# Performance work log

Hardware: AMD Instinct MI355X
Metric: run time of the kernel (lower is better)

The kernel has to match this reference:

```python
import jax, jax.numpy as jnp
import numpy as np

B, T, D, M = 4, 4096, 1024, 1024
EPS = 1e-6


def _rms_norm(x, w):
    return x * jax.lax.rsqrt(jnp.mean(x * x, axis=-1, keepdims=True) + EPS) * w


def _linrec(xg, r, h0):
    # h_t = x_t + r_t * h_{t-1}  (SRU-style linear recurrence, sqrll_kernel)
    def step(h, inp):
        xt, rt = inp
        h = xt + rt * h
        return h, h
    _, ys = jax.lax.scan(step, h0, (jnp.swapaxes(xg, 0, 1), jnp.swapaxes(r, 0, 1)))
    return jnp.swapaxes(ys, 0, 1)  # [B,T,M]


def setup_inputs() -> dict:
    key = jax.random.key(0)
    ks = jax.random.split(key, 16)
    s = 0.02
    return {
        "x": jax.random.normal(ks[0], (B, T, D), jnp.float32),
        "mem": jnp.zeros((B, M), jnp.float32),
        "norm_w": jnp.ones((D,), jnp.float32),
        "wr_w": jax.random.normal(ks[1], (M, D), jnp.float32) * s,
        "wr_b": jnp.zeros((M,), jnp.float32),
        "wi_w": jax.random.normal(ks[2], (M, D), jnp.float32) * s,
        "wig_w": jax.random.normal(ks[3], (M, D), jnp.float32) * s,
        "wig_b": jnp.zeros((M,), jnp.float32),
        "wog_w": jax.random.normal(ks[4], (M, D), jnp.float32) * s,
        "wog_b": jnp.zeros((M,), jnp.float32),
        "wo_w": jax.random.normal(ks[5], (D, M), jnp.float32) * s,
        "ffnorm_w": jnp.ones((D,), jnp.float32),
        "ffn_wi_w": jax.random.normal(ks[6], (M, D), jnp.float32) * s,
        "ffn_wg_w": jax.random.normal(ks[7], (M, D), jnp.float32) * s,
        "ffn_wg_b": jnp.zeros((M,), jnp.float32),
        "ffn_wo_w": jax.random.normal(ks[8], (D, M), jnp.float32) * s,
    }


def reference(x, mem, norm_w, wr_w, wr_b, wi_w, wig_w, wig_b, wog_w, wog_b,
              wo_w, ffnorm_w, ffn_wi_w, ffn_wg_w, ffn_wg_b, ffn_wo_w):
    # --- sqrll branch ---
    y = _rms_norm(x, norm_w)                                   # [B,T,D]
    ig = jax.nn.sigmoid(jnp.einsum('btd,md->btm', y, wig_w) + wig_b)
    og = jax.nn.sigmoid(jnp.einsum('btd,md->btm', y, wog_w) + wog_b)
    r = jax.nn.sigmoid(jnp.einsum('btd,md->btm', y, wr_w) + wr_b)
    xg = jnp.einsum('btd,md->btm', y, wi_w) * ig               # gated input
    h = _linrec(xg, r, mem)                                    # [B,T,M]
    mem_out = jax.lax.stop_gradient(h[:, -1])
    s = (h / (1.0 + jnp.abs(h))) * og                          # softsign * out gate
    x = x + jnp.einsum('btm,dm->btd', s, wo_w)                 # residual (dropout=0)
    # --- gated FFN branch ---
    z = _rms_norm(x, ffnorm_w)
    ff = jnp.einsum('btd,md->btm', z, ffn_wi_w) * jax.nn.sigmoid(
        jnp.einsum('btd,md->btm', z, ffn_wg_w) + ffn_wg_b)
    x = x + jnp.einsum('btm,dm->btd', ff, ffn_wo_w)
    return (x, mem_out)
```

## Files before the change

### kernel.cpp

```cpp
#include <hip/hip_runtime.h>
#include <stdint.h>


#define R_ROWS 16384
#define DIM    1024
#define MDIM   1024
#define TSEQ   4096
#define NCHUNK 128
#define TCH    32

typedef __attribute__((ext_vector_type(8))) short  bf16x8;
typedef __attribute__((ext_vector_type(8))) ushort u16x8;
typedef __attribute__((ext_vector_type(4))) float  f32x4;

__device__ __forceinline__ float bf2f(ushort u) {
  union { float f; unsigned int i; } x; x.i = ((unsigned int)u) << 16; return x.f;
}
__device__ __forceinline__ ushort f2bf(float f) {
  union { float f; unsigned int i; } x; x.f = f;
  unsigned int r = x.i + 0x7fffu + ((x.i >> 16) & 1u);
  return (ushort)(r >> 16);
}
__device__ __forceinline__ float sigmoidf_(float x) {
  return 1.0f / (1.0f + __expf(-x));
}
__device__ __forceinline__ void load_lds16(const void* g, void* s) {
  __builtin_amdgcn_global_load_lds(
      (const __attribute__((address_space(1))) void*)g,
      (__attribute__((address_space(3))) void*)s, 16, 0, 0);
}

__global__ __launch_bounds__(256)
void cvt_weights(const float* __restrict__ w0, const float* __restrict__ w1,
                 const float* __restrict__ w2, const float* __restrict__ w3,
                 const float* __restrict__ w4, const float* __restrict__ w5,
                 const float* __restrict__ w6, ushort* __restrict__ dst)
{
  const float* src;
  switch (blockIdx.y) {
    case 0: src = w0; break; case 1: src = w1; break;
    case 2: src = w2; break; case 3: src = w3; break;
    case 4: src = w4; break; case 5: src = w5; break;
    default: src = w6; break;
  }
  const int i = blockIdx.x * 256 + threadIdx.x;
  const size_t off = (size_t)blockIdx.y * 1048576 + (size_t)i * 4;
  const float4 v = *(const float4*)(src + (size_t)i * 4);
  ushort4 o; o.x = f2bf(v.x); o.y = f2bf(v.y); o.z = f2bf(v.z); o.w = f2bf(v.w);
  *(ushort4*)(dst + off) = o;
}

__global__ __launch_bounds__(256)
void cvt_one(const float* __restrict__ src, ushort* __restrict__ dst)
{
  const int i = blockIdx.x * 256 + threadIdx.x;
  const float4 v = *(const float4*)(src + (size_t)i * 4);
  ushort4 o; o.x = f2bf(v.x); o.y = f2bf(v.y); o.z = f2bf(v.z); o.w = f2bf(v.w);
  *(ushort4*)(dst + (size_t)i * 4) = o;
}

template<bool IN_F32>
__global__ __launch_bounds__(256)
void rmsnorm_k(const void* __restrict__ xin, const float* __restrict__ w,
               ushort* __restrict__ y)
{
  __shared__ float red[4];
  const int row = blockIdx.x;
  const int tid = threadIdx.x;
  const size_t base = (size_t)row * DIM + tid * 4;
  float v[4];
  if (IN_F32) {
    const float4 xv = *(const float4*)((const float*)xin + base);
    v[0] = xv.x; v[1] = xv.y; v[2] = xv.z; v[3] = xv.w;
  } else {
    const ushort4 xv = *(const ushort4*)((const ushort*)xin + base);
    v[0] = bf2f(xv.x); v[1] = bf2f(xv.y); v[2] = bf2f(xv.z); v[3] = bf2f(xv.w);
  }
  float ss = v[0]*v[0] + v[1]*v[1] + v[2]*v[2] + v[3]*v[3];
  for (int o = 32; o > 0; o >>= 1) ss += __shfl_down(ss, o, 64);
  const int wave = tid >> 6, lane = tid & 63;
  if (lane == 0) red[wave] = ss;
  __syncthreads();
  const float sum = red[0] + red[1] + red[2] + red[3];
  const float scale = rsqrtf(sum * (1.0f / DIM) + 1e-6f);
  const float4 wv = *(const float4*)(w + tid * 4);
  ushort4 o4;
  o4.x = f2bf(v[0] * scale * wv.x);
  o4.y = f2bf(v[1] * scale * wv.y);
  o4.z = f2bf(v[2] * scale * wv.z);
  o4.w = f2bf(v[3] * scale * wv.w);
  *(ushort4*)(y + base) = o4;
}

template<int MODE>
__global__ __launch_bounds__(512, 2)
void gemm8(const ushort* __restrict__ A, const ushort* __restrict__ W,
           const float* __restrict__ bias, const float* __restrict__ auxf,
           const ushort* __restrict__ auxb, ushort* __restrict__ outb,
           float* __restrict__ outf,
           const float* __restrict__ bias2, const float* __restrict__ bias3,
           ushort* __restrict__ outb2, ushort* __restrict__ outb3)
{
  __shared__ __align__(16) ushort lds[2][2][2][8192];
  const int tid  = threadIdx.x;
  const int bm = blockIdx.x, bn = blockIdx.y;
  const int wave = tid >> 6, lane = tid & 63;
  const int wm = wave >> 2, wn = wave & 3;
  const int quad = lane >> 4, l16 = lane & 15;
  const int axor = l16 & 7;

  const ushort* Ab = A + (size_t)bm * (256 * 1024);
  const ushort* Wb = W + (size_t)bn * (256 * 1024);

  f32x4 acc[8][4];
#pragma unroll
  for (int i = 0; i < 8; ++i)
#pragma unroll
    for (int j = 0; j < 4; ++j) acc[i][j] = (f32x4){0.f, 0.f, 0.f, 0.f};

  const int ci0 = tid, ci1 = tid + 512;
  const size_t gs0 = (size_t)(ci0 >> 3) * 1024 + (size_t)((((ci0 & 7) ^ ((ci0 >> 3) & 7))) << 3);
  const size_t gs1 = (size_t)(ci1 >> 3) * 1024 + (size_t)((((ci1 & 7) ^ ((ci1 >> 3) & 7))) << 3);
  auto stage = [&](const ushort* __restrict__ src, ushort* dst) {
    load_lds16(src + gs0, dst + ci0 * 8);
    load_lds16(src + gs1, dst + ci1 * 8);
  };

  stage(Ab,          &lds[0][0][0][0]); stage(Ab + 131072,      &lds[0][0][1][0]);
  stage(Wb,          &lds[0][1][0][0]); stage(Wb + 131072,      &lds[0][1][1][0]);
  stage(Wb + 64,     &lds[1][1][0][0]); stage(Wb + 131072 + 64, &lds[1][1][1][0]);
  asm volatile("s_waitcnt vmcnt(4)" ::: "memory");
  __builtin_amdgcn_s_barrier();

  for (int ktc = 0; ktc < 16; ++ktc) {
    const int b = ktc & 1;
    const ushort* Ah = &lds[b][0][wm][0];
    const ushort* Bh = &lds[b][1][wn >> 1][0];
    const int brow0 = (wn & 1) * 64;
    bf16x8 bfr[4][2];
#pragma unroll
    for (int q = 0; q < 4; ++q) {
      if (q == 0) {
#pragma unroll
        for (int j = 0; j < 4; ++j)
#pragma unroll
          for (int ks = 0; ks < 2; ++ks)
            bfr[j][ks] = *(const bf16x8*)
                &Bh[(brow0 + j * 16 + l16) * 64 +
                    (((ks * 4 + quad) ^ axor) << 3)];
      }
      bf16x8 af[2][2];
#pragma unroll
      for (int p = 0; p < 2; ++p)
#pragma unroll
        for (int ks = 0; ks < 2; ++ks)
          af[p][ks] = *(const bf16x8*)
              &Ah[((2 * q + p) * 16 + l16) * 64 +
                  (((ks * 4 + quad) ^ axor) << 3)];
      if (q == 0 && ktc + 1 < 16)
        stage(Ab + (ktc + 1) * 64, &lds[(ktc + 1) & 1][0][0][0]);
      if (q == 1 && ktc + 1 < 16)
        stage(Ab + 131072 + (ktc + 1) * 64, &lds[(ktc + 1) & 1][0][1][0]);
      if (q == 2 && ktc + 2 < 16)
        stage(Wb + (ktc + 2) * 64, &lds[ktc & 1][1][0][0]);
      if (q == 3 && ktc + 2 < 16)
        stage(Wb + 131072 + (ktc + 2) * 64, &lds[ktc & 1][1][1][0]);
      __builtin_amdgcn_s_barrier();
      asm volatile("s_waitcnt lgkmcnt(0)" ::: "memory");
      __builtin_amdgcn_s_setprio(1);
#pragma unroll
      for (int p = 0; p < 2; ++p)
#pragma unroll
        for (int j = 0; j < 4; ++j)
#pragma unroll
          for (int ks = 0; ks < 2; ++ks)
            acc[2 * q + p][j] = __builtin_amdgcn_mfma_f32_16x16x32_bf16(
                af[p][ks], bfr[j][ks], acc[2 * q + p][j], 0, 0, 0);
      __builtin_amdgcn_s_setprio(0);
      if (q == 3) {
        if (ktc >= 14) asm volatile("s_waitcnt vmcnt(0)" ::: "memory");
        else           asm volatile("s_waitcnt vmcnt(4)" ::: "memory");
      }
      __builtin_amdgcn_s_barrier();
    }
  }

  float* C = (float*)&lds[0][0][0][0];
  ushort* ob = outb;
  const float* bp = bias;
  int colbase = bn * 256;
  if (MODE == 4) {
    const int grp = bn >> 2;
    ob = (grp == 0) ? outb : (grp == 1) ? outb2 : outb3;
    bp = (grp == 0) ? bias : (grp == 1) ? bias2 : bias3;
    colbase = (bn & 3) * 256;
  }
#pragma unroll 1
  for (int h = 0; h < 2; ++h) {
    if (wm == h) {
      const int cb = wn * 64;
#pragma unroll
      for (int i = 0; i < 8; ++i)
#pragma unroll
        for (int j = 0; j < 4; ++j)
#pragma unroll
          for (int g = 0; g < 4; ++g) {
            const int rw = i * 16 + quad * 4 + g;
            const int cw = cb + j * 16 + l16;
            C[rw * 256 + (cw ^ (((rw >> 2) & 1) << 4))] = acc[i][j][g];
          }
    }
    __syncthreads();
#pragma unroll 1
    for (int sp = 0; sp < 8; ++sp) {
      const int lin = sp * 4096 + tid * 8;
      const int row = lin >> 8, c8 = lin & 255;
      const int xr = ((row >> 2) & 1) << 4;
      const int cx = c8 ^ xr;
      const float4 vA = *(const float4*)&C[row * 256 + cx];
      const float4 vB = *(const float4*)&C[row * 256 + cx + 4];
      const int rg = bm * 256 + h * 128 + row;
      const size_t gidx = (size_t)rg * 1024 + colbase + c8;
      if (MODE == 0 || MODE == 4) {
        const float4 b0 = *(const float4*)(bp + colbase + c8);
        const float4 b1 = *(const float4*)(bp + colbase + c8 + 4);
        u16x8 o;
        o[0] = f2bf(sigmoidf_(vA.x + b0.x)); o[1] = f2bf(sigmoidf_(vA.y + b0.y));
        o[2] = f2bf(sigmoidf_(vA.z + b0.z)); o[3] = f2bf(sigmoidf_(vA.w + b0.w));
        o[4] = f2bf(sigmoidf_(vB.x + b1.x)); o[5] = f2bf(sigmoidf_(vB.y + b1.y));
        o[6] = f2bf(sigmoidf_(vB.z + b1.z)); o[7] = f2bf(sigmoidf_(vB.w + b1.w));
        *(u16x8*)(ob + gidx) = o;
      } else if (MODE == 1) {
        const float4 a0 = *(const float4*)(auxf + gidx);
        const float4 a1 = *(const float4*)(auxf + gidx + 4);
        u16x8 o;
        o[0] = f2bf(vA.x + a0.x); o[1] = f2bf(vA.y + a0.y);
        o[2] = f2bf(vA.z + a0.z); o[3] = f2bf(vA.w + a0.w);
        o[4] = f2bf(vB.x + a1.x); o[5] = f2bf(vB.y + a1.y);
        o[6] = f2bf(vB.z + a1.z); o[7] = f2bf(vB.w + a1.w);
        *(u16x8*)(ob + gidx) = o;
      } else if (MODE == 2) {
        const u16x8 a8 = *(const u16x8*)(auxb + gidx);
        u16x8 o;
        o[0] = f2bf(vA.x * bf2f(a8[0])); o[1] = f2bf(vA.y * bf2f(a8[1]));
        o[2] = f2bf(vA.z * bf2f(a8[2])); o[3] = f2bf(vA.w * bf2f(a8[3]));
        o[4] = f2bf(vB.x * bf2f(a8[4])); o[5] = f2bf(vB.y * bf2f(a8[5]));
        o[6] = f2bf(vB.z * bf2f(a8[6])); o[7] = f2bf(vB.w * bf2f(a8[7]));
        *(u16x8*)(ob + gidx) = o;
      } else {
        const u16x8 a8 = *(const u16x8*)(auxb + gidx);
        float4 o0, o1;
        o0.x = vA.x + bf2f(a8[0]); o0.y = vA.y + bf2f(a8[1]);
        o0.z = vA.z + bf2f(a8[2]); o0.w = vA.w + bf2f(a8[3]);
        o1.x = vB.x + bf2f(a8[4]); o1.y = vB.y + bf2f(a8[5]);
        o1.z = vB.z + bf2f(a8[6]); o1.w = vB.w + bf2f(a8[7]);
        *(float4*)(outf + gidx) = o0;
        *(float4*)(outf + gidx + 4) = o1;
      }
    }
    if (h == 0) __syncthreads();
  }
}

__global__ __launch_bounds__(256)
void linrec_passA(ushort* __restrict__ xg, const ushort* __restrict__ r,
                  float* __restrict__ cL, float* __restrict__ cP)
{
  const int g = blockIdx.x * 256 + threadIdx.x;
  const int m4 = (g & 255) << 2;
  const int bc = g >> 8;
  const int b = bc >> 7, c = bc & 127;
  const size_t base = ((size_t)(b * TSEQ + c * TCH)) * MDIM + m4;
  float h0 = 0.f, h1 = 0.f, h2 = 0.f, h3 = 0.f;
  float p0 = 1.f, p1 = 1.f, p2 = 1.f, p3 = 1.f;
  for (int t = 0; t < TCH; ++t) {
    const size_t idx = base + (size_t)t * MDIM;
    const ushort4 xv = *(const ushort4*)&xg[idx];
    const ushort4 rv = *(const ushort4*)&r[idx];
    const float r0 = bf2f(rv.x), r1 = bf2f(rv.y), r2 = bf2f(rv.z), r3 = bf2f(rv.w);
    h0 = fmaf(r0, h0, bf2f(xv.x)); p0 *= r0;
    h1 = fmaf(r1, h1, bf2f(xv.y)); p1 *= r1;
    h2 = fmaf(r2, h2, bf2f(xv.z)); p2 *= r2;
    h3 = fmaf(r3, h3, bf2f(xv.w)); p3 *= r3;
    ushort4 o; o.x = f2bf(h0); o.y = f2bf(h1); o.z = f2bf(h2); o.w = f2bf(h3);
    *(ushort4*)&xg[idx] = o;
  }
  const size_t cb = (size_t)c * 4096 + b * MDIM + m4;
  float4 L4; L4.x = h0; L4.y = h1; L4.z = h2; L4.w = h3;
  float4 P4; P4.x = p0; P4.y = p1; P4.z = p2; P4.w = p3;
  *(float4*)&cL[cb] = L4;
  *(float4*)&cP[cb] = P4;
}

__global__ __launch_bounds__(256)
void linrec_passB(const float* __restrict__ cL, const float* __restrict__ cP,
                  const float* __restrict__ mem, float* __restrict__ cIn,
                  float* __restrict__ memout)
{
  const int g = blockIdx.x * 256 + threadIdx.x;
  float carry = mem[g];
#pragma unroll 4
  for (int c = 0; c < NCHUNK; ++c) {
    cIn[c * 4096 + g] = carry;
    carry = fmaf(cP[c * 4096 + g], carry, cL[c * 4096 + g]);
  }
  memout[g] = carry;
}

__global__ __launch_bounds__(256)
void linrec_passC(const ushort* __restrict__ L, const ushort* __restrict__ r,
                  const ushort* __restrict__ og, const float* __restrict__ cIn,
                  ushort* __restrict__ s)
{
  const int g = blockIdx.x * 256 + threadIdx.x;
  const int m4 = (g & 255) << 2;
  const int bc = g >> 8;
  const int b = bc >> 7, c = bc & 127;
  const size_t base = ((size_t)(b * TSEQ + c * TCH)) * MDIM + m4;
  const size_t cb = (size_t)c * 4096 + b * MDIM + m4;
  const float4 ci = *(const float4*)&cIn[cb];
  float p0 = 1.f, p1 = 1.f, p2 = 1.f, p3 = 1.f;
  for (int t = 0; t < TCH; ++t) {
    const size_t idx = base + (size_t)t * MDIM;
    const ushort4 rv = *(const ushort4*)&r[idx];
    const ushort4 lv = *(const ushort4*)&L[idx];
    const ushort4 ov = *(const ushort4*)&og[idx];
    p0 *= bf2f(rv.x); p1 *= bf2f(rv.y); p2 *= bf2f(rv.z); p3 *= bf2f(rv.w);
    const float a0 = fmaf(p0, ci.x, bf2f(lv.x));
    const float a1 = fmaf(p1, ci.y, bf2f(lv.y));
    const float a2 = fmaf(p2, ci.z, bf2f(lv.z));
    const float a3 = fmaf(p3, ci.w, bf2f(lv.w));
    ushort4 o;
    o.x = f2bf(a0 / (1.0f + fabsf(a0)) * bf2f(ov.x));
    o.y = f2bf(a1 / (1.0f + fabsf(a1)) * bf2f(ov.y));
    o.z = f2bf(a2 / (1.0f + fabsf(a2)) * bf2f(ov.z));
    o.w = f2bf(a3 / (1.0f + fabsf(a3)) * bf2f(ov.w));
    *(ushort4*)&s[idx] = o;
  }
}

extern "C" void kernel_launch(void* const* d_in, const int* in_sizes, int n_in,
                              void* d_out, int out_size, void* d_ws, size_t ws_size,
                              hipStream_t stream)
{
  const float* x        = (const float*)d_in[0];
  const float* mem      = (const float*)d_in[1];
  const float* norm_w   = (const float*)d_in[2];
  const float* wr_w     = (const float*)d_in[3];
  const float* wr_b     = (const float*)d_in[4];
  const float* wi_w     = (const float*)d_in[5];
  const float* wig_w    = (const float*)d_in[6];
  const float* wig_b    = (const float*)d_in[7];
  const float* wog_w    = (const float*)d_in[8];
  const float* wog_b    = (const float*)d_in[9];
  const float* wo_w     = (const float*)d_in[10];
  const float* ffnorm_w = (const float*)d_in[11];
  const float* ffn_wi_w = (const float*)d_in[12];
  const float* ffn_wg_w = (const float*)d_in[13];
  const float* ffn_wg_b = (const float*)d_in[14];
  const float* ffn_wo_w = (const float*)d_in[15];
  float* outF = (float*)d_out;

  ushort* xgL  = (ushort*)d_out;
  ushort* wbf  = (ushort*)((char*)d_out + 33554432ULL);
  float*  cL   = (float*)((char*)d_out + 48234496ULL);
  float*  cP   = (float*)((char*)d_out + 50331648ULL);
  float*  cIn  = (float*)((char*)d_out + 52428800ULL);
  float*  memoutF = outF + 16777216;

  char* ws = (char*)d_ws;
  ushort* y   = (ushort*)(ws);
  ushort* r   = (ushort*)(ws + 33554432ULL);
  ushort* og  = (ushort*)(ws + 67108864ULL);
  ushort* fwo_bf = (ushort*)(ws + 100663296ULL);
  ushort* s   = y;
  ushort* x1  = og;
  ushort* z   = r;
  ushort* gf  = y;

  ushort* wr_bf   = wbf + 0 * 1048576;
  ushort* wi_bf   = wbf + 3 * 1048576;
  ushort* wo_bf   = wbf + 4 * 1048576;
  ushort* fwi_bf  = wbf + 5 * 1048576;
  ushort* fwg_bf  = wbf + 6 * 1048576;

  const dim3 g8(64, 4);
  const dim3 g83(64, 12);

  cvt_weights<<<dim3(1024, 7), 256, 0, stream>>>(
      wr_w, wog_w, wig_w, wi_w, wo_w, ffn_wi_w, ffn_wg_w, wbf);
  cvt_one<<<1024, 256, 0, stream>>>(ffn_wo_w, fwo_bf);

  rmsnorm_k<true><<<R_ROWS, 256, 0, stream>>>(x, norm_w, y);
  gemm8<4><<<g83, 512, 0, stream>>>(y, wr_bf, wr_b, nullptr, nullptr, r, nullptr,
                                    wog_b, wig_b, og, xgL);
  gemm8<2><<<g8, 512, 0, stream>>>(y, wi_bf, nullptr, nullptr, xgL, xgL, nullptr,
                                   nullptr, nullptr, nullptr, nullptr);
  linrec_passA<<<512, 256, 0, stream>>>(xgL, r, cL, cP);
  linrec_passB<<<16, 256, 0, stream>>>(cL, cP, mem, cIn, memoutF);
  linrec_passC<<<512, 256, 0, stream>>>(xgL, r, og, cIn, s);
  gemm8<1><<<g8, 512, 0, stream>>>(s, wo_bf, nullptr, x, nullptr, x1, nullptr,
                                   nullptr, nullptr, nullptr, nullptr);
  rmsnorm_k<false><<<R_ROWS, 256, 0, stream>>>(x1, ffnorm_w, z);
  gemm8<0><<<g8, 512, 0, stream>>>(z, fwg_bf, ffn_wg_b, nullptr, nullptr, gf, nullptr,
                                   nullptr, nullptr, nullptr, nullptr);
  gemm8<2><<<g8, 512, 0, stream>>>(z, fwi_bf, nullptr, nullptr, gf, gf, nullptr,
                                   nullptr, nullptr, nullptr, nullptr);
  gemm8<3><<<g8, 512, 0, stream>>>(gf, fwo_bf, nullptr, nullptr, x1, nullptr, outF,
                                   nullptr, nullptr, nullptr, nullptr);
}
```

Baseline: 556.3 us.

## Fuse gated GEMM pairs via interleaved weights and triple-buffer A tiles

Weight conversion now interleaves the gate and value weight matrices in 128-row blocks. A single GEMM tile can then compute both the gate and value columns and apply value*sigmoid(gate+bias) in its epilogue. This folds the input-gate/wi pair into the wr/wog launch and the FFN gate/wi pair into one launch, so the intermediate bf16 gate tensors are no longer written and re-read. The K-loop also changes from double to triple buffering of A in LDS, with a reordered staging schedule and one barrier per sub-step instead of two. The cost is more LDS per block (160KB), which may limit occupancy.

```diff
diff --git a/kernel.cpp b/kernel.cpp
--- a/kernel.cpp
+++ b/kernel.cpp
@@ -30,22 +30,35 @@
       (__attribute__((address_space(3))) void*)s, 16, 0, 0);
 }
 
+#define AOFF(s,h) ((((s)*2)+(h))*8192)
+#define BOFF(s,h) (49152 + (((s)*2)+(h))*8192)
+
 __global__ __launch_bounds__(256)
 void cvt_weights(const float* __restrict__ w0, const float* __restrict__ w1,
                  const float* __restrict__ w2, const float* __restrict__ w3,
                  const float* __restrict__ w4, const float* __restrict__ w5,
                  const float* __restrict__ w6, ushort* __restrict__ dst)
 {
-  const float* src;
+  const float* src; size_t base; int il;
   switch (blockIdx.y) {
-    case 0: src = w0; break; case 1: src = w1; break;
-    case 2: src = w2; break; case 3: src = w3; break;
-    case 4: src = w4; break; case 5: src = w5; break;
-    default: src = w6; break;
+    case 0: src = w0; base = 0;       il = 0; break;
+    case 1: src = w1; base = 1048576; il = 0; break;
+    case 2: src = w2; base = 2097152; il = 1; break;
+    case 3: src = w3; base = 2097152; il = 2; break;
+    case 4: src = w4; base = 5242880; il = 1; break;
+    case 5: src = w5; base = 5242880; il = 2; break;
+    default: src = w6; base = 4194304; il = 0; break;
   }
   const int i = blockIdx.x * 256 + threadIdx.x;
-  const size_t off = (size_t)blockIdx.y * 1048576 + (size_t)i * 4;
-  const float4 v = *(const float4*)(src + (size_t)i * 4);
+  const size_t e = (size_t)i * 4;
+  size_t off;
+  if (il == 0) off = base + e;
+  else {
+    const int row = (int)(e >> 10), col = (int)(e & 1023);
+    const int nr = ((row >> 7) << 8) + (row & 127) + (il == 2 ? 128 : 0);
+    off = base + (size_t)nr * 1024 + col;
+  }
+  const float4 v = *(const float4*)(src + e);
   ushort4 o; o.x = f2bf(v.x); o.y = f2bf(v.y); o.z = f2bf(v.z); o.w = f2bf(v.w);
   *(ushort4*)(dst + off) = o;
 }
@@ -101,7 +114,7 @@
            const float* __restrict__ bias2, const float* __restrict__ bias3,
            ushort* __restrict__ outb2, ushort* __restrict__ outb3)
 {
-  __shared__ __align__(16) ushort lds[2][2][2][8192];
+  __shared__ __align__(16) ushort lds[81920];
   const int tid  = threadIdx.x;
   const int bm = blockIdx.x, bn = blockIdx.y;
   const int wave = tid >> 6, lane = tid & 63;
@@ -119,23 +132,28 @@
     for (int j = 0; j < 4; ++j) acc[i][j] = (f32x4){0.f, 0.f, 0.f, 0.f};
 
   const int ci0 = tid, ci1 = tid + 512;
-  const size_t gs0 = (size_t)(ci0 >> 3) * 1024 + (size_t)((((ci0 & 7) ^ ((ci0 >> 3) & 7))) << 3);
-  const size_t gs1 = (size_t)(ci1 >> 3) * 1024 + (size_t)((((ci1 & 7) ^ ((ci1 >> 3) & 7))) << 3);
-  auto stage = [&](const ushort* __restrict__ src, ushort* dst) {
-    load_lds16(src + gs0, dst + ci0 * 8);
-    load_lds16(src + gs1, dst + ci1 * 8);
+  const size_t gs0 = (size_t)(ci0 >> 3) * 1024 + (size_t)(((ci0 & 7) ^ ((ci0 >> 3) & 7)) << 3);
+  const size_t gs1 = (size_t)(ci1 >> 3) * 1024 + (size_t)(((ci1 & 7) ^ ((ci1 >> 3) & 7)) << 3);
+  auto stage = [&](const ushort* __restrict__ src, int loff) {
+    load_lds16(src + gs0, &lds[loff + ci0 * 8]);
+    load_lds16(src + gs1, &lds[loff + ci1 * 8]);
   };
 
-  stage(Ab,          &lds[0][0][0][0]); stage(Ab + 131072,      &lds[0][0][1][0]);
-  stage(Wb,          &lds[0][1][0][0]); stage(Wb + 131072,      &lds[0][1][1][0]);
-  stage(Wb + 64,     &lds[1][1][0][0]); stage(Wb + 131072 + 64, &lds[1][1][1][0]);
-  asm volatile("s_waitcnt vmcnt(4)" ::: "memory");
+  stage(Ab,               AOFF(0,0));
+  stage(Ab + 131072,      AOFF(0,1));
+  stage(Wb,               BOFF(0,0));
+  stage(Wb + 131072,      BOFF(0,1));
+  stage(Ab + 64,          AOFF(1,0));
+  stage(Ab + 131072 + 64, AOFF(1,1));
+  stage(Wb + 64,          BOFF(1,0));
+  asm volatile("s_waitcnt vmcnt(6)" ::: "memory");
   __builtin_amdgcn_s_barrier();
 
-  for (int ktc = 0; ktc < 16; ++ktc) {
-    const int b = ktc & 1;
-    const ushort* Ah = &lds[b][0][wm][0];
-    const ushort* Bh = &lds[b][1][wn >> 1][0];
+  int kt3 = 0;
+  for (int kt = 0; kt < 16; ++kt) {
+    const ushort* Ah = &lds[AOFF(kt3, wm)];
+    const ushort* Bh = &lds[BOFF(kt & 1, wn >> 1)];
+    const int kt2s = (kt3 >= 1) ? kt3 - 1 : 2;
     const int brow0 = (wn & 1) * 64;
     bf16x8 bfr[4][2];
 #pragma unroll
@@ -157,14 +175,18 @@
           af[p][ks] = *(const bf16x8*)
               &Ah[((2 * q + p) * 16 + l16) * 64 +
                   (((ks * 4 + quad) ^ axor) << 3)];
-      if (q == 0 && ktc + 1 < 16)
-        stage(Ab + (ktc + 1) * 64, &lds[(ktc + 1) & 1][0][0][0]);
-      if (q == 1 && ktc + 1 < 16)
-        stage(Ab + 131072 + (ktc + 1) * 64, &lds[(ktc + 1) & 1][0][1][0]);
-      if (q == 2 && ktc + 2 < 16)
-        stage(Wb + (ktc + 2) * 64, &lds[ktc & 1][1][0][0]);
-      if (q == 3 && ktc + 2 < 16)
-        stage(Wb + 131072 + (ktc + 2) * 64, &lds[ktc & 1][1][1][0]);
+      if (q == 0 && kt + 1 < 16)
+        stage(Wb + 131072 + (kt + 1) * 64, BOFF((kt + 1) & 1, 1));
+      if (q == 1 && kt + 2 < 16)
+        stage(Ab + (kt + 2) * 64,          AOFF(kt2s, 0));
+      if (q == 2 && kt + 2 < 16)
+        stage(Ab + 131072 + (kt + 2) * 64, AOFF(kt2s, 1));
+      if (q == 3) {
+        if (kt + 2 < 16)
+          stage(Wb + (kt + 2) * 64,        BOFF(kt & 1, 0));
+        if (kt < 14)       asm volatile("s_waitcnt vmcnt(6)" ::: "memory");
+        else if (kt == 14) asm volatile("s_waitcnt vmcnt(0)" ::: "memory");
+      }
       __builtin_amdgcn_s_barrier();
       asm volatile("s_waitcnt lgkmcnt(0)" ::: "memory");
       __builtin_amdgcn_s_setprio(1);
@@ -177,24 +199,13 @@
             acc[2 * q + p][j] = __builtin_amdgcn_mfma_f32_16x16x32_bf16(
                 af[p][ks], bfr[j][ks], acc[2 * q + p][j], 0, 0, 0);
       __builtin_amdgcn_s_setprio(0);
-      if (q == 3) {
-        if (ktc >= 14) asm volatile("s_waitcnt vmcnt(0)" ::: "memory");
-        else           asm volatile("s_waitcnt vmcnt(4)" ::: "memory");
-      }
-      __builtin_amdgcn_s_barrier();
     }
-  }
-
-  float* C = (float*)&lds[0][0][0][0];
-  ushort* ob = outb;
-  const float* bp = bias;
-  int colbase = bn * 256;
-  if (MODE == 4) {
-    const int grp = bn >> 2;
-    ob = (grp == 0) ? outb : (grp == 1) ? outb2 : outb3;
-    bp = (grp == 0) ? bias : (grp == 1) ? bias2 : bias3;
-    colbase = (bn & 3) * 256;
-  }
+    kt3 = (kt3 == 2) ? 0 : kt3 + 1;
+  }
+
+  __builtin_amdgcn_s_barrier();
+  float* C = (float*)lds;
+  const bool gated = (MODE == 5) || (MODE == 6 && bn >= 8);
 #pragma unroll 1
   for (int h = 0; h < 2; ++h) {
     if (wm == h) {
@@ -211,51 +222,81 @@
           }
     }
     __syncthreads();
+    if (gated) {
+      const int outcol = (MODE == 6) ? (bn - 8) * 128 : bn * 128;
+      const float* bp = (MODE == 6) ? bias3 : bias;
+      ushort* ob = (MODE == 6) ? outb3 : outb;
 #pragma unroll 1
-    for (int sp = 0; sp < 8; ++sp) {
-      const int lin = sp * 4096 + tid * 8;
-      const int row = lin >> 8, c8 = lin & 255;
-      const int xr = ((row >> 2) & 1) << 4;
-      const int cx = c8 ^ xr;
-      const float4 vA = *(const float4*)&C[row * 256 + cx];
-      const float4 vB = *(const float4*)&C[row * 256 + cx + 4];
-      const int rg = bm * 256 + h * 128 + row;
-      const size_t gidx = (size_t)rg * 1024 + colbase + c8;
-      if (MODE == 0 || MODE == 4) {
-        const float4 b0 = *(const float4*)(bp + colbase + c8);
-        const float4 b1 = *(const float4*)(bp + colbase + c8 + 4);
+      for (int sp = 0; sp < 4; ++sp) {
+        const int lin = sp * 4096 + tid * 8;
+        const int row = lin >> 7, c8 = lin & 127;
+        const int xr = ((row >> 2) & 1) << 4;
+        const int cg = c8 ^ xr;
+        const int cv = (c8 + 128) ^ xr;
+        const float4 gA = *(const float4*)&C[row * 256 + cg];
+        const float4 gB = *(const float4*)&C[row * 256 + cg + 4];
+        const float4 vA = *(const float4*)&C[row * 256 + cv];
+        const float4 vB = *(const float4*)&C[row * 256 + cv + 4];
+        const float4 b0 = *(const float4*)(bp + outcol + c8);
+        const float4 b1 = *(const float4*)(bp + outcol + c8 + 4);
+        const int rg = bm * 256 + h * 128 + row;
+        const size_t gidx = (size_t)rg * 1024 + outcol + c8;
         u16x8 o;
-        o[0] = f2bf(sigmoidf_(vA.x + b0.x)); o[1] = f2bf(sigmoidf_(vA.y + b0.y));
-        o[2] = f2bf(sigmoidf_(vA.z + b0.z)); o[3] = f2bf(sigmoidf_(vA.w + b0.w));
-        o[4] = f2bf(sigmoidf_(vB.x + b1.x)); o[5] = f2bf(sigmoidf_(vB.y + b1.y));
-        o[6] = f2bf(sigmoidf_(vB.z + b1.z)); o[7] = f2bf(sigmoidf_(vB.w + b1.w));
+        o[0] = f2bf(vA.x * sigmoidf_(gA.x + b0.x));
+        o[1] = f2bf(vA.y * sigmoidf_(gA.y + b0.y));
+        o[2] = f2bf(vA.z * sigmoidf_(gA.z + b0.z));
+        o[3] = f2bf(vA.w * sigmoidf_(gA.w + b0.w));
+        o[4] = f2bf(vB.x * sigmoidf_(gB.x + b1.x));
+        o[5] = f2bf(vB.y * sigmoidf_(gB.y + b1.y));
+        o[6] = f2bf(vB.z * sigmoidf_(gB.z + b1.z));
+        o[7] = f2bf(vB.w * sigmoidf_(gB.w + b1.w));
         *(u16x8*)(ob + gidx) = o;
-      } else if (MODE == 1) {
-        const float4 a0 = *(const float4*)(auxf + gidx);
-        const float4 a1 = *(const float4*)(auxf + gidx + 4);
-        u16x8 o;
-        o[0] = f2bf(vA.x + a0.x); o[1] = f2bf(vA.y + a0.y);
-        o[2] = f2bf(vA.z + a0.z); o[3] = f2bf(vA.w + a0.w);
-        o[4] = f2bf(vB.x + a1.x); o[5] = f2bf(vB.y + a1.y);
-        o[6] = f2bf(vB.z + a1.z); o[7] = f2bf(vB.w + a1.w);
-        *(u16x8*)(ob + gidx) = o;
-      } else if (MODE == 2) {
-        const u16x8 a8 = *(const u16x8*)(auxb + gidx);
-        u16x8 o;
-        o[0] = f2bf(vA.x * bf2f(a8[0])); o[1] = f2bf(vA.y * bf2f(a8[1]));
-        o[2] = f2bf(vA.z * bf2f(a8[2])); o[3] = f2bf(vA.w * bf2f(a8[3]));
-        o[4] = f2bf(vB.x * bf2f(a8[4])); o[5] = f2bf(vB.y * bf2f(a8[5]));
-        o[6] = f2bf(vB.z * bf2f(a8[6])); o[7] = f2bf(vB.w * bf2f(a8[7]));
-        *(u16x8*)(ob + gidx) = o;
-      } else {
-        const u16x8 a8 = *(const u16x8*)(auxb + gidx);
-        float4 o0, o1;
-        o0.x = vA.x + bf2f(a8[0]); o0.y = vA.y + bf2f(a8[1]);
-        o0.z = vA.z + bf2f(a8[2]); o0.w = vA.w + bf2f(a8[3]);
-        o1.x = vB.x + bf2f(a8[4]); o1.y = vB.y + bf2f(a8[5]);
-        o1.z = vB.z + bf2f(a8[6]); o1.w = vB.w + bf2f(a8[7]);
-        *(float4*)(outf + gidx) = o0;
-        *(float4*)(outf + gidx + 4) = o1;
+      }
+    } else {
+#pragma unroll 1
+      for (int sp = 0; sp < 8; ++sp) {
+        const int lin = sp * 4096 + tid * 8;
+        const int row = lin >> 8, c8 = lin & 255;
+        const int xr = ((row >> 2) & 1) << 4;
+        const int cx = c8 ^ xr;
+        const float4 vA = *(const float4*)&C[row * 256 + cx];
+        const float4 vB = *(const float4*)&C[row * 256 + cx + 4];
+        const int rg = bm * 256 + h * 128 + row;
+        if (MODE == 6) {
+          const int grp = bn >> 2;
+          ushort* ob = grp ? outb2 : outb;
+          const float* bp = grp ? bias2 : bias;
+          const int colbase = (bn & 3) * 256;
+          const size_t gidx = (size_t)rg * 1024 + colbase + c8;
+          const float4 b0 = *(const float4*)(bp + colbase + c8);
+          const float4 b1 = *(const float4*)(bp + colbase + c8 + 4);
+          u16x8 o;
+          o[0] = f2bf(sigmoidf_(vA.x + b0.x)); o[1] = f2bf(sigmoidf_(vA.y + b0.y));
+          o[2] = f2bf(sigmoidf_(vA.z + b0.z)); o[3] = f2bf(sigmoidf_(vA.w + b0.w));
+          o[4] = f2bf(sigmoidf_(vB.x + b1.x)); o[5] = f2bf(sigmoidf_(vB.y + b1.y));
+          o[6] = f2bf(sigmoidf_(vB.z + b1.z)); o[7] = f2bf(sigmoidf_(vB.w + b1.w));
+          *(u16x8*)(ob + gidx) = o;
+        } else if (MODE == 1) {
+          const size_t gidx = (size_t)rg * 1024 + bn * 256 + c8;
+          const float4 a0 = *(const float4*)(auxf + gidx);
+          const float4 a1 = *(const float4*)(auxf + gidx + 4);
+          u16x8 o;
+          o[0] = f2bf(vA.x + a0.x); o[1] = f2bf(vA.y + a0.y);
+          o[2] = f2bf(vA.z + a0.z); o[3] = f2bf(vA.w + a0.w);
+          o[4] = f2bf(vB.x + a1.x); o[5] = f2bf(vB.y + a1.y);
+          o[6] = f2bf(vB.z + a1.z); o[7] = f2bf(vB.w + a1.w);
+          *(u16x8*)(outb + gidx) = o;
+        } else {
+          const size_t gidx = (size_t)rg * 1024 + bn * 256 + c8;
+          const u16x8 a8 = *(const u16x8*)(auxb + gidx);
+          float4 o0, o1;
+          o0.x = vA.x + bf2f(a8[0]); o0.y = vA.y + bf2f(a8[1]);
+          o0.z = vA.z + bf2f(a8[2]); o0.w = vA.w + bf2f(a8[3]);
+          o1.x = vB.x + bf2f(a8[4]); o1.y = vB.y + bf2f(a8[5]);
+          o1.z = vB.z + bf2f(a8[6]); o1.w = vB.w + bf2f(a8[7]);
+          *(float4*)(outf + gidx) = o0;
+          *(float4*)(outf + gidx + 4) = o1;
+        }
       }
     }
     if (h == 0) __syncthreads();
@@ -378,34 +419,24 @@
   ushort* z   = r;
   ushort* gf  = y;
 
-  ushort* wr_bf   = wbf + 0 * 1048576;
-  ushort* wi_bf   = wbf + 3 * 1048576;
-  ushort* wo_bf   = wbf + 4 * 1048576;
-  ushort* fwi_bf  = wbf + 5 * 1048576;
-  ushort* fwg_bf  = wbf + 6 * 1048576;
-
-  const dim3 g8(64, 4);
-  const dim3 g83(64, 12);
-
   cvt_weights<<<dim3(1024, 7), 256, 0, stream>>>(
-      wr_w, wog_w, wig_w, wi_w, wo_w, ffn_wi_w, ffn_wg_w, wbf);
+      wr_w, wog_w, wig_w, wi_w, ffn_wg_w, ffn_wi_w, wo_w, wbf);
   cvt_one<<<1024, 256, 0, stream>>>(ffn_wo_w, fwo_bf);
 
   rmsnorm_k<true><<<R_ROWS, 256, 0, stream>>>(x, norm_w, y);
-  gemm8<4><<<g83, 512, 0, stream>>>(y, wr_bf, wr_b, nullptr, nullptr, r, nullptr,
-                                    wog_b, wig_b, og, xgL);
-  gemm8<2><<<g8, 512, 0, stream>>>(y, wi_bf, nullptr, nullptr, xgL, xgL, nullptr,
-                                   nullptr, nullptr, nullptr, nullptr);
+  gemm8<6><<<dim3(64, 16), 512, 0, stream>>>(
+      y, wbf, wr_b, nullptr, nullptr, r, nullptr, wog_b, wig_b, og, xgL);
   linrec_passA<<<512, 256, 0, stream>>>(xgL, r, cL, cP);
   linrec_passB<<<16, 256, 0, stream>>>(cL, cP, mem, cIn, memoutF);
   linrec_passC<<<512, 256, 0, stream>>>(xgL, r, og, cIn, s);
-  gemm8<1><<<g8, 512, 0, stream>>>(s, wo_bf, nullptr, x, nullptr, x1, nullptr,
-                                   nullptr, nullptr, nullptr, nullptr);
+  gemm8<1><<<dim3(64, 4), 512, 0, stream>>>(
+      s, wbf + 4194304, nullptr, x, nullptr, x1, nullptr,
+      nullptr, nullptr, nullptr, nullptr);
   rmsnorm_k<false><<<R_ROWS, 256, 0, stream>>>(x1, ffnorm_w, z);
-  gemm8<0><<<g8, 512, 0, stream>>>(z, fwg_bf, ffn_wg_b, nullptr, nullptr, gf, nullptr,
-                                   nullptr, nullptr, nullptr, nullptr);
-  gemm8<2><<<g8, 512, 0, stream>>>(z, fwi_bf, nullptr, nullptr, gf, gf, nullptr,
-                                   nullptr, nullptr, nullptr, nullptr);
-  gemm8<3><<<g8, 512, 0, stream>>>(gf, fwo_bf, nullptr, nullptr, x1, nullptr, outF,
-                                   nullptr, nullptr, nullptr, nullptr);
-}
+  gemm8<5><<<dim3(64, 8), 512, 0, stream>>>(
+      z, wbf + 5242880, ffn_wg_b, nullptr, nullptr, gf, nullptr,
+      nullptr, nullptr, nullptr, nullptr);
+  gemm8<3><<<dim3(64, 4), 512, 0, stream>>>(
+      gf, fwo_bf, nullptr, nullptr, x1, nullptr, outF,
+      nullptr, nullptr, nullptr, nullptr);
+}
```

New measurement: 530.1 us. 4.7% less time.
